# Optimization experiments

Hardware: AMD Instinct MI355X
Metric: run time of the kernel (lower is better)

## Reference

```python
import jax, jax.numpy as jnp
import numpy as np

B, T, C = 64, 512, 384
H = 6
HD = C // H  # 64
FF = 4 * C
EPS = 1e-5


def _rope(x):
    # x: [B,H,T,D]. Faithful to source: fres = 1/1000^(arange(0,D,2)//D) == all ones
    # (integer floor division), so the rotation angle is just the position t.
    t = jnp.arange(x.shape[2], dtype=jnp.float32)
    cos = jnp.cos(t)[None, None, :, None]
    sin = jnp.sin(t)[None, None, :, None]
    xr = x[..., 0::2]
    xi = x[..., 1::2]
    outr = cos * xr - sin * xi
    outi = sin * xr + cos * xi
    return jnp.stack([outr, outi], axis=-1).reshape(x.shape)


def _mha(x, qw, qb, kw, kb, vw, vb, pw, pb):
    # per-head projections batched over H: [B,T,C] x [H,C,D] -> [B,H,T,D]
    q = jnp.einsum('btc,hcd->bhtd', x, qw) + qb[None, :, None, :]
    k = jnp.einsum('btc,hcd->bhtd', x, kw) + kb[None, :, None, :]
    v = jnp.einsum('btc,hcd->bhtd', x, vw) + vb[None, :, None, :]
    q = _rope(q)
    k = _rope(k)
    # NOTE: source scales by C**-0.5 with C = n_embed (384), not head_size.
    wei = jnp.einsum('bhtd,bhsd->bhts', q, k) * (C ** -0.5)
    Tq = x.shape[1]
    causal = jnp.tril(jnp.ones((Tq, Tq), dtype=bool))
    wei = jnp.where(causal[None, None], wei, -jnp.inf)
    wei = jax.nn.softmax(wei, axis=-1)
    out = jnp.einsum('bhts,bhsd->bhtd', wei, v)
    out = out.transpose(0, 2, 1, 3).reshape(x.shape[0], Tq, C)  # concat heads
    return out @ pw + pb


def _ln(x, g, b):
    m = jnp.mean(x, axis=-1, keepdims=True)
    var = jnp.mean((x - m) ** 2, axis=-1, keepdims=True)
    return g * (x - m) / jnp.sqrt(var + EPS) + b


def setup_inputs() -> dict:
    key = jax.random.key(0)
    ks = jax.random.split(key, 16)
    s = 0.02
    d = {
        'x': jax.random.normal(ks[0], (B, T, C), dtype=jnp.float32),
        'q1_w': jax.random.normal(ks[1], (H, C, HD)) * s, 'q1_b': jnp.zeros((H, HD)),
        'k1_w': jax.random.normal(ks[2], (H, C, HD)) * s, 'k1_b': jnp.zeros((H, HD)),
        'v1_w': jax.random.normal(ks[3], (H, C, HD)) * s, 'v1_b': jnp.zeros((H, HD)),
        'p1_w': jax.random.normal(ks[4], (C, C)) * s, 'p1_b': jnp.zeros((C,)),
        'ln1_g': jnp.ones((C,)), 'ln1_b': jnp.zeros((C,)),
        'q2_w': jax.random.normal(ks[5], (H, C, HD)) * s, 'q2_b': jnp.zeros((H, HD)),
        'k2_w': jax.random.normal(ks[6], (H, C, HD)) * s, 'k2_b': jnp.zeros((H, HD)),
        'v2_w': jax.random.normal(ks[7], (H, C, HD)) * s, 'v2_b': jnp.zeros((H, HD)),
        'p2_w': jax.random.normal(ks[8], (C, C)) * s, 'p2_b': jnp.zeros((C,)),
        'ln2_g': jnp.ones((C,)), 'ln2_b': jnp.zeros((C,)),
        'f1_w': jax.random.normal(ks[9], (C, FF)) * s, 'f1_b': jnp.zeros((FF,)),
        'f2_w': jax.random.normal(ks[10], (FF, C)) * s, 'f2_b': jnp.zeros((C,)),
        'ln3_g': jnp.ones((C,)), 'ln3_b': jnp.zeros((C,)),
    }
    return {k2: jnp.asarray(v, jnp.float32) for k2, v in d.items()}


def reference(x, q1_w, q1_b, k1_w, k1_b, v1_w, v1_b, p1_w, p1_b, ln1_g, ln1_b,
              q2_w, q2_b, k2_w, k2_b, v2_w, v2_b, p2_w, p2_b, ln2_g, ln2_b,
              f1_w, f1_b, f2_w, f2_b, ln3_g, ln3_b):
    attn1 = _mha(x, q1_w, q1_b, k1_w, k1_b, v1_w, v1_b, p1_w, p1_b)
    out1 = _ln(x + attn1, ln1_g, ln1_b)
    attn2 = _mha(out1, q2_w, q2_b, k2_w, k2_b, v2_w, v2_b, p2_w, p2_b)
    out2 = _ln(out1 + attn2, ln2_g, ln2_b)
    ff = jax.nn.relu(out2 @ f1_w + f1_b) @ f2_w + f2_b
    return _ln(out2 + ff, ln3_g, ln3_b)
```

## Files before the change

kernel.cpp:

```cpp
#include <hip/hip_runtime.h>
#include <cstddef>
#include <cstdint>

#define B_ 64
#define T_ 512
#define C_ 384
#define H_ 6
#define HD_ 64
#define FF_ 1536

typedef unsigned short u16;
typedef unsigned int u32;
typedef __attribute__((ext_vector_type(8))) __bf16 bf16x8;
typedef __attribute__((ext_vector_type(8))) short short8;
typedef __attribute__((ext_vector_type(4))) float f32x4;

#define MFMA_BF16(a, b, c) __builtin_amdgcn_mfma_f32_16x16x32_bf16((a), (b), (c), 0, 0, 0)

__device__ __forceinline__ u16 f2bf(float f) {
    union { float f; unsigned u; } x; x.f = f;
    unsigned r = x.u + 0x7fff + ((x.u >> 16) & 1);
    return (u16)(r >> 16);
}

__device__ __forceinline__ void gload16(const u16* g, u16* l) {
    __builtin_amdgcn_global_load_lds(
        (const __attribute__((address_space(1))) void*)g,
        (__attribute__((address_space(3))) void*)l, 16, 0, 0);
}

__device__ __forceinline__ int swz4(int row, int ch) { return ch ^ ((row >> 1) & 3); }

__global__ __launch_bounds__(256)
void prep_kernel(const float* __restrict__ q1w, const float* __restrict__ k1w, const float* __restrict__ v1w,
                 const float* __restrict__ q2w, const float* __restrict__ k2w, const float* __restrict__ v2w,
                 const float* __restrict__ p1w, const float* __restrict__ p2w,
                 const float* __restrict__ f1w, const float* __restrict__ f2w,
                 const float* __restrict__ q1b, const float* __restrict__ k1b, const float* __restrict__ v1b,
                 const float* __restrict__ q2b, const float* __restrict__ k2b, const float* __restrict__ v2b,
                 u16* wq1, u16* wq2, u16* p1t, u16* p2t, u16* f1t, u16* f2t,
                 float* bq1, float* bq2, float* cst, float* snt)
{
    const int job = blockIdx.y;
    const int idx = blockIdx.x * 256 + threadIdx.x;
    if (job <= 1) {
        if (idx >= 1152 * 384) return;
        const int n = idx / 384, k = idx - n * 384;
        const int wsel = n / 384;
        const int rest = n - wsel * 384;
        const int h = rest >> 6, d = rest & 63;
        const float* src;
        if (job == 0) src = (wsel == 0 ? q1w : wsel == 1 ? k1w : v1w);
        else          src = (wsel == 0 ? q2w : wsel == 1 ? k2w : v2w);
        (job == 0 ? wq1 : wq2)[idx] = f2bf(src[((size_t)h * 384 + k) * 64 + d]);
    } else if (job <= 3) {
        if (idx >= 384 * 384) return;
        const int n = idx / 384, k = idx - n * 384;
        const float* src = (job == 2 ? p1w : p2w);
        (job == 2 ? p1t : p2t)[idx] = f2bf(src[(size_t)k * 384 + n]);
    } else if (job == 4) {
        if (idx >= 1536 * 384) return;
        const int n = idx / 384, k = idx - n * 384;
        f1t[idx] = f2bf(f1w[(size_t)k * 1536 + n]);
    } else if (job == 5) {
        if (idx >= 384 * 1536) return;
        const int n = idx / 1536, k = idx - n * 1536;
        f2t[idx] = f2bf(f2w[(size_t)k * 384 + n]);
    } else {
        if (idx < 1152) {
            const int wsel = idx / 384, r = idx - wsel * 384;
            bq1[idx] = (wsel == 0 ? q1b : wsel == 1 ? k1b : v1b)[r];
        } else if (idx < 2304) {
            const int j = idx - 1152;
            const int wsel = j / 384, r = j - wsel * 384;
            bq2[j] = (wsel == 0 ? q2b : wsel == 1 ? k2b : v2b)[r];
        } else if (idx < 2816) {
            const int t = idx - 2304; cst[t] = cosf((float)t);
        } else if (idx < 3328) {
            const int t = idx - 2816; snt[t] = sinf((float)t);
        }
    }
}

__global__ __launch_bounds__(256)
void cast_kernel(const float* __restrict__ in, u16* __restrict__ out, int n4)
{
    int i = blockIdx.x * 256 + threadIdx.x;
    const int stride = gridDim.x * 256;
    for (; i < n4; i += stride) {
        float4 v = *reinterpret_cast<const float4*>(&in[(size_t)i * 4]);
        ushort4 o;
        o.x = f2bf(v.x); o.y = f2bf(v.y); o.z = f2bf(v.z); o.w = f2bf(v.w);
        *reinterpret_cast<ushort4*>(&out[(size_t)i * 4]) = o;
    }
}

template<int EPI>
__global__ __launch_bounds__(256)
void gemm_mfma(const u16* __restrict__ A, const u16* __restrict__ Bt, int K,
               const float* __restrict__ bias, const float* __restrict__ res,
               float* __restrict__ outf, u16* __restrict__ outb,
               u16* __restrict__ qo, u16* __restrict__ ko, u16* __restrict__ vo,
               const float* __restrict__ cst, const float* __restrict__ snt,
               int N)
{
    __shared__ u16 As[2][128 * 32];
    __shared__ u16 Bs[2][128 * 32];
    const int tid = threadIdx.x;
    const int w = tid >> 6, lane = tid & 63;
    const int m0 = blockIdx.x * 128, n0 = blockIdx.y * 128;
    const int wm = w >> 1, wn = w & 1;
    const int c = lane & 15, g = lane >> 4;
    const int cs = (c >> 1) & 3;

    const int srow = w * 16 + (lane >> 2);
    const u16* gA = A + (size_t)(m0 + srow) * K + swz4(srow, lane & 3) * 8;
    const u16* gB = Bt + (size_t)(n0 + srow) * K + swz4(srow, lane & 3) * 8;
    const int ldst = w * 512;

    f32x4 acc[4][4];
    #pragma unroll
    for (int i = 0; i < 4; ++i)
        #pragma unroll
        for (int j = 0; j < 4; ++j) acc[i][j] = (f32x4)0.0f;

    const int NT = K >> 5;

    gload16(gA, As[0] + ldst);
    gload16(gA + (size_t)64 * K, As[0] + 64 * 32 + ldst);
    gload16(gB, Bs[0] + ldst);
    gload16(gB + (size_t)64 * K, Bs[0] + 64 * 32 + ldst);
    __syncthreads();

    for (int t = 0; t < NT; ++t) {
        const int cur = t & 1;
        if (t + 1 < NT) {
            const int k0 = (t + 1) * 32;
            gload16(gA + k0, As[cur ^ 1] + ldst);
            gload16(gA + k0 + (size_t)64 * K, As[cur ^ 1] + 64 * 32 + ldst);
            gload16(gB + k0, Bs[cur ^ 1] + ldst);
            gload16(gB + k0 + (size_t)64 * K, Bs[cur ^ 1] + 64 * 32 + ldst);
        }
        bf16x8 af[4], bfr[4];
        #pragma unroll
        for (int fi = 0; fi < 4; ++fi)
            af[fi] = *(const bf16x8*)&As[cur][(wm * 64 + fi * 16 + c) * 32 + (g ^ cs) * 8];
        #pragma unroll
        for (int fj = 0; fj < 4; ++fj)
            bfr[fj] = *(const bf16x8*)&Bs[cur][(wn * 64 + fj * 16 + c) * 32 + (g ^ cs) * 8];
        #pragma unroll
        for (int fi = 0; fi < 4; ++fi)
            #pragma unroll
            for (int fj = 0; fj < 4; ++fj)
                acc[fi][fj] = MFMA_BF16(af[fi], bfr[fj], acc[fi][fj]);
        __syncthreads();
    }

    if (EPI == 0) {
        const int which = blockIdx.y / 3;
        u16* dst = (which == 0 ? qo : which == 1 ? ko : vo);
        #pragma unroll
        for (int fi = 0; fi < 4; ++fi) {
            #pragma unroll
            for (int r = 0; r < 4; ++r) {
                const int m = m0 + wm * 64 + fi * 16 + 4 * g + r;
                const int t = m & 511, bb = m >> 9;
                const float csn = cst[t], sn = snt[t];
                #pragma unroll
                for (int fj = 0; fj < 4; ++fj) {
                    const int n = n0 + wn * 64 + fj * 16 + c;
                    float v = acc[fi][fj][r] + bias[n];
                    const float vp = __shfl_xor(v, 1);
                    float ov;
                    if (which < 2)
                        ov = ((n & 1) == 0) ? csn * v - sn * vp : sn * vp + csn * v;
                    else
                        ov = v;
                    const float op = __shfl_xor(ov, 1);
                    if ((c & 1) == 0) {
                        const int rest = n - which * 384;
                        const int h = rest >> 6, d = rest & 63;
                        const u32 pk = (u32)f2bf(ov) | ((u32)f2bf(op) << 16);
                        *(u32*)&dst[(((size_t)bb * H_ + h) * T_ + t) * 64 + d] = pk;
                    }
                }
            }
        }
    } else if (EPI == 1) {
        #pragma unroll
        for (int fi = 0; fi < 4; ++fi) {
            #pragma unroll
            for (int r = 0; r < 4; ++r) {
                const int m = m0 + wm * 64 + fi * 16 + 4 * g + r;
                #pragma unroll
                for (int fj = 0; fj < 4; ++fj) {
                    const int n = n0 + wn * 64 + fj * 16 + c;
                    float v = acc[fi][fj][r] + bias[n] + res[(size_t)m * N + n];
                    outf[(size_t)m * N + n] = v;
                }
            }
        }
    } else {
        #pragma unroll
        for (int fi = 0; fi < 4; ++fi) {
            #pragma unroll
            for (int r = 0; r < 4; ++r) {
                const int m = m0 + wm * 64 + fi * 16 + 4 * g + r;
                #pragma unroll
                for (int fj = 0; fj < 4; ++fj) {
                    const int n = n0 + wn * 64 + fj * 16 + c;
                    float v = fmaxf(acc[fi][fj][r] + bias[n], 0.0f);
                    const float vn = __shfl_xor(v, 1);
                    if ((c & 1) == 0) {
                        const u32 pk = (u32)f2bf(v) | ((u32)f2bf(vn) << 16);
                        *(u32*)&outb[(size_t)m * N + n] = pk;
                    }
                }
            }
        }
    }
}

#define KS_B(r, chB) ((r) * 176 + (chB) * 16)
#define VT_B(d, t)   ((d) * 176 + ((((t) >> 3) ^ ((d) & 7) ^ ((d) >> 3)) << 4) + (((t) & 7) << 1))

__global__ __launch_bounds__(256)
void attn_mfma(const u16* __restrict__ Q, const u16* __restrict__ K,
               const u16* __restrict__ V, u16* __restrict__ out)
{
    __shared__ u16 Ks[64 * 88];
    __shared__ u16 Vt[64 * 88];
    __shared__ u16 Ps[4][16 * 88];

    const int qt = blockIdx.x, h = blockIdx.y, b = blockIdx.z;
    const int tid = threadIdx.x;
    const int w = tid >> 6, lane = tid & 63;
    const int c = lane & 15, g = lane >> 4;
    const size_t base = ((size_t)b * H_ + h) * T_ * 64;
    const int qrow0 = qt * 64 + w * 16;
    const float scale = 0.05103103630798288f;

    bf16x8 qf[2];
    #pragma unroll
    for (int kh = 0; kh < 2; ++kh)
        qf[kh] = *(const bf16x8*)&Q[base + (size_t)(qrow0 + c) * 64 + kh * 32 + g * 8];

    f32x4 O[4];
    float m_[4], l_[4];
    #pragma unroll
    for (int i = 0; i < 4; ++i) { O[i] = (f32x4)0.0f; m_[i] = -INFINITY; l_[i] = 0.0f; }

    u16* Pw = Ps[w];

    for (int kt = 0; kt <= qt; ++kt) {
        __syncthreads();
        #pragma unroll
        for (int s = 0; s < 2; ++s) {
            const int idx = tid + s * 256;
            const int r = idx >> 3, ch = idx & 7;
            const size_t gsrc = base + (size_t)(kt * 64 + r) * 64 + ch * 8;
            short8 kv = *(const short8*)&K[gsrc];
            *(short8*)((char*)Ks + KS_B(r, ch)) = kv;
            short8 vv = *(const short8*)&V[gsrc];
            #pragma unroll
            for (int j = 0; j < 8; ++j)
                *(u16*)((char*)Vt + VT_B(ch * 8 + j, r)) = (u16)vv[j];
        }
        __syncthreads();

        f32x4 S[4];
        #pragma unroll
        for (int fc = 0; fc < 4; ++fc) {
            S[fc] = (f32x4)0.0f;
            #pragma unroll
            for (int kh = 0; kh < 2; ++kh) {
                bf16x8 kf = *(const bf16x8*)((char*)Ks + KS_B(fc * 16 + c, kh * 4 + g));
                S[fc] = MFMA_BF16(qf[kh], kf, S[fc]);
            }
        }

        const bool diag = (kt == qt);
        #pragma unroll
        for (int r = 0; r < 4; ++r) {
            const int qloc = w * 16 + 4 * g + r;
            float mx = -INFINITY;
            #pragma unroll
            for (int fc = 0; fc < 4; ++fc) {
                float sv = S[fc][r] * scale;
                if (diag && (fc * 16 + c > qloc)) sv = -INFINITY;
                S[fc][r] = sv;
                mx = fmaxf(mx, sv);
            }
            #pragma unroll
            for (int off = 1; off < 16; off <<= 1)
                mx = fmaxf(mx, __shfl_xor(mx, off, 16));
            const float mnew = fmaxf(m_[r], mx);
            const float corr = __expf(m_[r] - mnew);
            m_[r] = mnew;
            float su = 0.0f;
            #pragma unroll
            for (int fc = 0; fc < 4; ++fc) {
                const float p = __expf(S[fc][r] - mnew);
                S[fc][r] = p; su += p;
            }
            #pragma unroll
            for (int off = 1; off < 16; off <<= 1)
                su += __shfl_xor(su, off, 16);
            l_[r] = l_[r] * corr + su;
            #pragma unroll
            for (int fd = 0; fd < 4; ++fd) O[fd][r] *= corr;
        }

        #pragma unroll
        for (int fc = 0; fc < 4; ++fc)
            #pragma unroll
            for (int r = 0; r < 4; ++r)
                *(u16*)((char*)Pw + (4 * g + r) * 176 + (fc * 16 + c) * 2) = f2bf(S[fc][r]);

        bf16x8 pa[2];
        #pragma unroll
        for (int kh = 0; kh < 2; ++kh)
            pa[kh] = *(const bf16x8*)((char*)Pw + c * 176 + kh * 64 + g * 16);
        #pragma unroll
        for (int fd = 0; fd < 4; ++fd) {
            const int d = fd * 16 + c;
            #pragma unroll
            for (int kh = 0; kh < 2; ++kh) {
                const int kb = kh * 4 + g;
                bf16x8 vf = *(const bf16x8*)((char*)Vt + d * 176 + (((kb) ^ (d & 7) ^ (d >> 3)) << 4));
                O[fd] = MFMA_BF16(pa[kh], vf, O[fd]);
            }
        }
    }

    #pragma unroll
    for (int r = 0; r < 4; ++r) {
        const int t = qrow0 + 4 * g + r;
        const float inv = 1.0f / l_[r];
        const size_t o = ((size_t)b * T_ + t) * C_ + h * 64;
        #pragma unroll
        for (int fd = 0; fd < 4; ++fd)
            out[o + fd * 16 + c] = f2bf(O[fd][r] * inv);
    }
}

__global__ __launch_bounds__(256)
void ln_kernel(const float* __restrict__ in, const float* __restrict__ gam,
               const float* __restrict__ bta, float* __restrict__ outf,
               u16* __restrict__ outb)
{
    const int lane = threadIdx.x & 63;
    const int wv   = threadIdx.x >> 6;
    const size_t row = (size_t)blockIdx.x * 4 + wv;
    const float* x = in + row * C_;

    float vals[6];
    float s = 0.0f;
    #pragma unroll
    for (int i = 0; i < 6; ++i) { vals[i] = x[lane + i * 64]; s += vals[i]; }
    #pragma unroll
    for (int off = 1; off < 64; off <<= 1) s += __shfl_xor(s, off, 64);
    const float mean = s * (1.0f / 384.0f);

    float vs = 0.0f;
    #pragma unroll
    for (int i = 0; i < 6; ++i) { const float d = vals[i] - mean; vs += d * d; }
    #pragma unroll
    for (int off = 1; off < 64; off <<= 1) vs += __shfl_xor(vs, off, 64);
    const float inv = rsqrtf(vs * (1.0f / 384.0f) + 1e-5f);

    #pragma unroll
    for (int i = 0; i < 6; ++i) {
        const int cc = lane + i * 64;
        const float y = gam[cc] * (vals[i] - mean) * inv + bta[cc];
        if (outf) outf[row * C_ + cc] = y;
        if (outb) outb[row * C_ + cc] = f2bf(y);
    }
}

extern "C" void kernel_launch(void* const* d_in, const int* in_sizes, int n_in,
                              void* d_out, int out_size, void* d_ws, size_t ws_size,
                              hipStream_t stream)
{
    const float* x    = (const float*)d_in[0];
    const float* q1w  = (const float*)d_in[1];  const float* q1b = (const float*)d_in[2];
    const float* k1w  = (const float*)d_in[3];  const float* k1b = (const float*)d_in[4];
    const float* v1w  = (const float*)d_in[5];  const float* v1b = (const float*)d_in[6];
    const float* p1w  = (const float*)d_in[7];  const float* p1b = (const float*)d_in[8];
    const float* ln1g = (const float*)d_in[9];  const float* ln1b = (const float*)d_in[10];
    const float* q2w  = (const float*)d_in[11]; const float* q2b = (const float*)d_in[12];
    const float* k2w  = (const float*)d_in[13]; const float* k2b = (const float*)d_in[14];
    const float* v2w  = (const float*)d_in[15]; const float* v2b = (const float*)d_in[16];
    const float* p2w  = (const float*)d_in[17]; const float* p2b = (const float*)d_in[18];
    const float* ln2g = (const float*)d_in[19]; const float* ln2b = (const float*)d_in[20];
    const float* f1w  = (const float*)d_in[21]; const float* f1b = (const float*)d_in[22];
    const float* f2w  = (const float*)d_in[23]; const float* f2b = (const float*)d_in[24];
    const float* ln3g = (const float*)d_in[25]; const float* ln3b = (const float*)d_in[26];

    const size_t WQKV = 1152 * 384, WP = 384 * 384, WF = 1536 * 384;
    u16* wq1 = (u16*)d_ws;
    u16* wq2 = wq1 + WQKV;
    u16* p1t = wq2 + WQKV;
    u16* p2t = p1t + WP;
    u16* f1t = p2t + WP;
    u16* f2t = f1t + WF;
    float* bq1 = (float*)(f2t + WF);
    float* bq2 = bq1 + 1152;
    float* cst = bq2 + 1152;
    float* snt = cst + 512;
    u16* chunkBase = (u16*)(snt + 512);
    const size_t fixedBytes = (size_t)((char*)chunkBase - (char*)d_ws);

    int CB = 64;
    while (CB > 1 && fixedBytes + 20ull * CB * T_ * C_ > ws_size) CB >>= 1;
    const size_t McC = (size_t)CB * T_ * C_;
    const int Mc = CB * T_;

    u16* sQ  = chunkBase;
    u16* sK  = sQ + McC;
    u16* sV  = sK + McC;
    u16* sAb = sV + McC;
    u16* sX  = sAb + McC;
    u16* sO2 = sX + McC;
    u16* tmp = sQ;
    float* bufF = (float*)(sO2 + McC);
    float* y1f  = bufF + McC;

    const dim3 blk(256);

    prep_kernel<<<dim3(2304, 7), blk, 0, stream>>>(
        q1w, k1w, v1w, q2w, k2w, v2w, p1w, p2w, f1w, f2w,
        q1b, k1b, v1b, q2b, k2b, v2b,
        wq1, wq2, p1t, p2t, f1t, f2t, bq1, bq2, cst, snt);

    for (int b0 = 0; b0 < B_; b0 += CB) {
        const float* xc = x + (size_t)b0 * T_ * C_;
        float*       oc = (float*)d_out + (size_t)b0 * T_ * C_;

        cast_kernel<<<dim3(2048), blk, 0, stream>>>(xc, sX, (int)(McC / 4));

        gemm_mfma<0><<<dim3(Mc / 128, 9), blk, 0, stream>>>(sX, wq1, 384, bq1,
            nullptr, nullptr, nullptr, sQ, sK, sV, cst, snt, 1152);
        attn_mfma<<<dim3(T_ / 64, H_, CB), blk, 0, stream>>>(sQ, sK, sV, sAb);
        gemm_mfma<1><<<dim3(Mc / 128, 3), blk, 0, stream>>>(sAb, p1t, 384, p1b,
            xc, bufF, nullptr, nullptr, nullptr, nullptr, cst, snt, 384);
        ln_kernel<<<dim3(Mc / 4), blk, 0, stream>>>(bufF, ln1g, ln1b, y1f, sX);

        gemm_mfma<0><<<dim3(Mc / 128, 9), blk, 0, stream>>>(sX, wq2, 384, bq2,
            nullptr, nullptr, nullptr, sQ, sK, sV, cst, snt, 1152);
        attn_mfma<<<dim3(T_ / 64, H_, CB), blk, 0, stream>>>(sQ, sK, sV, sAb);
        gemm_mfma<1><<<dim3(Mc / 128, 3), blk, 0, stream>>>(sAb, p2t, 384, p2b,
            y1f, bufF, nullptr, nullptr, nullptr, nullptr, cst, snt, 384);
        ln_kernel<<<dim3(Mc / 4), blk, 0, stream>>>(bufF, ln2g, ln2b, oc, sO2);

        gemm_mfma<2><<<dim3(Mc / 128, 12), blk, 0, stream>>>(sO2, f1t, 384, f1b,
            nullptr, nullptr, tmp, nullptr, nullptr, nullptr, cst, snt, 1536);
        gemm_mfma<1><<<dim3(Mc / 128, 3), blk, 0, stream>>>(tmp, f2t, 1536, f2b,
            oc, bufF, nullptr, nullptr, nullptr, nullptr, cst, snt, 384);
        ln_kernel<<<dim3(Mc / 4), blk, 0, stream>>>(bufF, ln3g, ln3b, oc, nullptr);
    }
}
```

Baseline: 814.6 us.

## Prefetch next K/V tile into registers and remap attention blocks across XCDs

The attention kernel now loads the next K/V tile from global memory into registers before computing the current tile, and writes it to shared memory afterward, so load latency overlaps with MFMA work. V transposition is packed as two rows per 32-bit store, and P is written as packed bf16 pairs using a lane shuffle. The grid is flattened and block IDs are remapped so consecutive hardware blocks (likely round-robined over 8 XCDs) share a head/batch and its K/V in cache. The prefetch adds register pressure and still needs two barriers per iteration.

```diff
diff --git a/kernel.cpp b/kernel.cpp
--- a/kernel.cpp
+++ b/kernel.cpp
@@ -226,16 +226,23 @@
 
 __global__ __launch_bounds__(256)
 void attn_mfma(const u16* __restrict__ Q, const u16* __restrict__ K,
-               const u16* __restrict__ V, u16* __restrict__ out)
+               const u16* __restrict__ V, u16* __restrict__ out, int cpx)
 {
     __shared__ u16 Ks[64 * 88];
     __shared__ u16 Vt[64 * 88];
     __shared__ u16 Ps[4][16 * 88];
 
-    const int qt = blockIdx.x, h = blockIdx.y, b = blockIdx.z;
+    const int wg = blockIdx.x;
+    const int logical = (wg & 7) * cpx + (wg >> 3);
+    const int qt = logical & 7;
+    const int hb = logical >> 3;
+    const int h = hb % H_, b = hb / H_;
+
     const int tid = threadIdx.x;
     const int w = tid >> 6, lane = tid & 63;
     const int c = lane & 15, g = lane >> 4;
+    const int p2 = tid >> 3;
+    const int ch = tid & 7;
     const size_t base = ((size_t)b * H_ + h) * T_ * 64;
     const int qrow0 = qt * 64 + w * 16;
     const float scale = 0.05103103630798288f;
@@ -252,21 +259,32 @@
 
     u16* Pw = Ps[w];
 
+    {
+        const size_t src = base + (size_t)(2 * p2) * 64 + ch * 8;
+        short8 krA = *(const short8*)&K[src];
+        short8 krB = *(const short8*)&K[src + 64];
+        short8 vrA = *(const short8*)&V[src];
+        short8 vrB = *(const short8*)&V[src + 64];
+        *(short8*)((char*)Ks + KS_B(2 * p2, ch)) = krA;
+        *(short8*)((char*)Ks + KS_B(2 * p2 + 1, ch)) = krB;
+        #pragma unroll
+        for (int j = 0; j < 8; ++j) {
+            const int d = ch * 8 + j;
+            const u32 pk = (u32)(u16)vrA[j] | ((u32)(u16)vrB[j] << 16);
+            *(u32*)((char*)Vt + VT_B(d, 2 * p2)) = pk;
+        }
+    }
+    __syncthreads();
+
+    short8 krA, krB, vrA, vrB;
     for (int kt = 0; kt <= qt; ++kt) {
-        __syncthreads();
-        #pragma unroll
-        for (int s = 0; s < 2; ++s) {
-            const int idx = tid + s * 256;
-            const int r = idx >> 3, ch = idx & 7;
-            const size_t gsrc = base + (size_t)(kt * 64 + r) * 64 + ch * 8;
-            short8 kv = *(const short8*)&K[gsrc];
-            *(short8*)((char*)Ks + KS_B(r, ch)) = kv;
-            short8 vv = *(const short8*)&V[gsrc];
-            #pragma unroll
-            for (int j = 0; j < 8; ++j)
-                *(u16*)((char*)Vt + VT_B(ch * 8 + j, r)) = (u16)vv[j];
-        }
-        __syncthreads();
+        if (kt < qt) {
+            const size_t src = base + (size_t)((kt + 1) * 64 + 2 * p2) * 64 + ch * 8;
+            krA = *(const short8*)&K[src];
+            krB = *(const short8*)&K[src + 64];
+            vrA = *(const short8*)&V[src];
+            vrB = *(const short8*)&V[src + 64];
+        }
 
         f32x4 S[4];
         #pragma unroll
@@ -314,8 +332,14 @@
         #pragma unroll
         for (int fc = 0; fc < 4; ++fc)
             #pragma unroll
-            for (int r = 0; r < 4; ++r)
-                *(u16*)((char*)Pw + (4 * g + r) * 176 + (fc * 16 + c) * 2) = f2bf(S[fc][r]);
+            for (int r = 0; r < 4; ++r) {
+                const float pv = S[fc][r];
+                const float pn = __shfl_xor(pv, 1);
+                if ((c & 1) == 0) {
+                    const u32 pk = (u32)f2bf(pv) | ((u32)f2bf(pn) << 16);
+                    *(u32*)((char*)Pw + (4 * g + r) * 176 + (fc * 16 + c) * 2) = pk;
+                }
+            }
 
         bf16x8 pa[2];
         #pragma unroll
@@ -330,6 +354,19 @@
                 bf16x8 vf = *(const bf16x8*)((char*)Vt + d * 176 + (((kb) ^ (d & 7) ^ (d >> 3)) << 4));
                 O[fd] = MFMA_BF16(pa[kh], vf, O[fd]);
             }
+        }
+
+        if (kt < qt) {
+            __syncthreads();
+            *(short8*)((char*)Ks + KS_B(2 * p2, ch)) = krA;
+            *(short8*)((char*)Ks + KS_B(2 * p2 + 1, ch)) = krB;
+            #pragma unroll
+            for (int j = 0; j < 8; ++j) {
+                const int d = ch * 8 + j;
+                const u32 pk = (u32)(u16)vrA[j] | ((u32)(u16)vrB[j] << 16);
+                *(u32*)((char*)Vt + VT_B(d, 2 * p2)) = pk;
+            }
+            __syncthreads();
         }
     }
 
@@ -427,6 +464,8 @@
     float* y1f  = bufF + McC;
 
     const dim3 blk(256);
+    const int attnBlocks = 48 * CB;
+    const int cpx = 6 * CB;
 
     prep_kernel<<<dim3(2304, 7), blk, 0, stream>>>(
         q1w, k1w, v1w, q2w, k2w, v2w, p1w, p2w, f1w, f2w,
@@ -441,14 +480,14 @@
 
         gemm_mfma<0><<<dim3(Mc / 128, 9), blk, 0, stream>>>(sX, wq1, 384, bq1,
             nullptr, nullptr, nullptr, sQ, sK, sV, cst, snt, 1152);
-        attn_mfma<<<dim3(T_ / 64, H_, CB), blk, 0, stream>>>(sQ, sK, sV, sAb);
+        attn_mfma<<<dim3(attnBlocks), blk, 0, stream>>>(sQ, sK, sV, sAb, cpx);
         gemm_mfma<1><<<dim3(Mc / 128, 3), blk, 0, stream>>>(sAb, p1t, 384, p1b,
             xc, bufF, nullptr, nullptr, nullptr, nullptr, cst, snt, 384);
         ln_kernel<<<dim3(Mc / 4), blk, 0, stream>>>(bufF, ln1g, ln1b, y1f, sX);
 
         gemm_mfma<0><<<dim3(Mc / 128, 9), blk, 0, stream>>>(sX, wq2, 384, bq2,
             nullptr, nullptr, nullptr, sQ, sK, sV, cst, snt, 1152);
-        attn_mfma<<<dim3(T_ / 64, H_, CB), blk, 0, stream>>>(sQ, sK, sV, sAb);
+        attn_mfma<<<dim3(attnBlocks), blk, 0, stream>>>(sQ, sK, sV, sAb, cpx);
         gemm_mfma<1><<<dim3(Mc / 128, 3), blk, 0, stream>>>(sAb, p2t, 384, p2b,
             y1f, bufF, nullptr, nullptr, nullptr, nullptr, cst, snt, 384);
         ln_kernel<<<dim3(Mc / 4), blk, 0, stream>>>(bufF, ln2g, ln2b, oc, sO2);
```

New measurement: 803.2 us. Within noise of the previous version (-1.4%).
